# Kernel tuning notes

Measured on AMD Instinct MI355X. Metric: run time of the kernel, lower is better.

Reference implementation:

```python
import jax, jax.numpy as jnp
import numpy as np
import math

N_ENT = 200000
N_USERS = 100000
N_FACTORS = 4
N_REL = 26
CH = 64
N_EDGES = 1000000
NNZ = 1000000
KG_HEADS = 2


def scatter_softmax(scores, seg, num_segments):
    # numerically-stable softmax over groups defined by seg (per-head softmax)
    m = jax.ops.segment_max(scores, seg, num_segments=num_segments)
    m = jnp.where(jnp.isfinite(m), m, 0.0)
    e = jnp.exp(scores - m[seg])
    d = jax.ops.segment_sum(e, seg, num_segments=num_segments)
    return e / d[seg]


def setup_inputs() -> dict:
    key = jax.random.key(0)
    ks = jax.random.split(key, 11)
    return {
        "entity_emb": jax.random.normal(ks[0], (N_ENT, CH), dtype=jnp.float32) * 0.1,
        "user_emb": jax.random.normal(ks[1], (N_USERS, CH), dtype=jnp.float32) * 0.1,
        "latent_emb": jax.random.normal(ks[2], (N_FACTORS, CH), dtype=jnp.float32) * 0.1,
        "edge_index": jax.random.randint(ks[3], (2, N_EDGES), 0, N_ENT),
        "edge_type": jax.random.randint(ks[4], (N_EDGES,), 1, N_REL),  # in [1, N_REL-1]
        "ui_rows": jax.random.randint(ks[5], (NNZ,), 0, N_USERS),
        "ui_cols": jax.random.randint(ks[6], (NNZ,), 0, N_ENT),
        "ui_vals": jax.random.uniform(ks[7], (NNZ,), dtype=jnp.float32),
        "weight": jax.random.normal(ks[8], (N_REL - 1, CH), dtype=jnp.float32) * 0.1,
        "disen_weight_att": jax.random.normal(ks[9], (N_FACTORS, N_REL - 1), dtype=jnp.float32) * 0.1,
        "kg_W_r": jax.random.normal(ks[10], (CH, CH), dtype=jnp.float32) * (1.0 / math.sqrt(CH)),
    }


def reference(entity_emb, user_emb, latent_emb, edge_index, edge_type,
              ui_rows, ui_cols, ui_vals, weight, disen_weight_att, kg_W_r):
    head, tail = edge_index[0], edge_index[1]
    d_k = CH // KG_HEADS

    # --- Invariant_Capture.relation_aware_att ---
    rel_emb = weight[edge_type - 1]            # [E, C] gather
    h_emb = entity_emb[head]                   # [E, C] gather
    q = (h_emb @ kg_W_r).reshape(-1, KG_HEADS, d_k)
    k = (rel_emb @ kg_W_r).reshape(-1, KG_HEADS, d_k)
    score_r = ((q * k).sum(-1) / math.sqrt(d_k)).mean(-1)   # [E]
    rel_attn = scatter_softmax(score_r, head, N_ENT)

    # --- Invariant_Capture.kg_inv_capture ---
    t_emb = entity_emb[tail]                   # [E, C] gather
    r_emb = rel_emb * rel_attn[:, None]
    # bmm(cat(h,r), cat(t,r)^T) == h.t + r.r per edge
    score_trip = (h_emb * t_emb).sum(-1) + (r_emb * r_emb).sum(-1)
    kg_mask = scatter_softmax(score_trip, head, N_ENT)       # invariant_mask [E]

    # --- Aggregator: KG scatter-mean with invariant mask ---
    neigh = t_emb * rel_emb * kg_mask[:, None]               # [E, C]
    sums = jax.ops.segment_sum(neigh, head, num_segments=N_ENT)
    cnt = jax.ops.segment_sum(jnp.ones((neigh.shape[0],), dtype=neigh.dtype), head, num_segments=N_ENT)
    entity_agg = sums / jnp.maximum(cnt, 1.0)[:, None]       # scatter_mean

    # --- Aggregator: user side ---
    score = jax.nn.softmax(user_emb @ latent_emb.T, axis=1)  # [U, F]
    user_agg = jax.ops.segment_sum(entity_emb[ui_cols] * ui_vals[:, None], ui_rows, num_segments=N_USERS)
    disen_weight = jax.nn.softmax(disen_weight_att, axis=-1) @ weight  # [F, C]
    # (expand(U,F,C) * score[:,:,None]).sum(1) == score @ disen_weight
    user_agg = user_agg * (score @ disen_weight) + user_agg

    return jnp.concatenate([entity_agg, user_agg], axis=0)   # [N_ENT+N_USERS, C]
```

## Files before the change

kernel.cpp:

```cpp
#include <hip/hip_runtime.h>
#include <math.h>

#define N_ENT 200000
#define N_USERS 100000
#define NKEY 300000
#define N_FACTORS 4
#define NREL1 25
#define CH 64
#define N_EDGES 1000000
#define NNZ 1000000
#define NREC 2000000
#define BSHIFT 11
#define BKEYS 2048
#define NBUCKET 147
#define TILE 2048
#define CAP 24576
#define NCONVB ((N_ENT * 8 + 1023) / 1024)

#define SCORE_SCALE 0.08838834764831845f
#define INV_Q14 6.103888176768602e-05f

__device__ __forceinline__ float red8(float d) {
    d += __shfl_xor(d, 1);
    d += __shfl_xor(d, 2);
    d += __shfl_xor(d, 4);
    return d;
}
__device__ __forceinline__ float dot4(float4 a, float4 b) {
    return a.x * b.x + a.y * b.y + a.z * b.z + a.w * b.w;
}
__device__ __forceinline__ unsigned short f2bf(float f) {
    unsigned u = __float_as_uint(f);
    u += 0x7FFFu + ((u >> 16) & 1u);
    return (unsigned short)(u >> 16);
}
__device__ __forceinline__ float bf2f(unsigned short u) {
    return __uint_as_float(((unsigned)u) << 16);
}
__device__ __forceinline__ float4 bf4lo(uint4 t) {
    return make_float4(__uint_as_float(t.x << 16), __uint_as_float(t.x & 0xFFFF0000u),
                       __uint_as_float(t.y << 16), __uint_as_float(t.y & 0xFFFF0000u));
}
__device__ __forceinline__ float4 bf4hi(uint4 t) {
    return make_float4(__uint_as_float(t.z << 16), __uint_as_float(t.z & 0xFFFF0000u),
                       __uint_as_float(t.w << 16), __uint_as_float(t.w & 0xFFFF0000u));
}

__global__ void precompute_k(const float* __restrict__ W,
                             const float* __restrict__ weight,
                             const float* __restrict__ datt,
                             float* __restrict__ Mvec,
                             float* __restrict__ wnorm,
                             float* __restrict__ disen) {
    __shared__ float sW[64 * 64];
    __shared__ float sw[NREL1 * 64];
    __shared__ float sWWt[64 * 64];
    int tid = threadIdx.x;
    for (int i = tid; i < 64 * 64; i += 256) sW[i] = W[i];
    for (int i = tid; i < NREL1 * 64; i += 256) sw[i] = weight[i];
    __syncthreads();
    for (int e = tid; e < 64 * 64; e += 256) {
        int i = e >> 6, j = e & 63;
        float s = 0.f;
        for (int k = 0; k < 64; ++k) s += sW[i * 64 + k] * sW[j * 64 + k];
        sWWt[e] = s;
    }
    __syncthreads();
    for (int e = tid; e < NREL1 * 64; e += 256) {
        int r = e >> 6, i = e & 63;
        float s = 0.f;
        for (int j = 0; j < 64; ++j) s += sWWt[i * 64 + j] * sw[r * 64 + j];
        Mvec[e] = s;
    }
    for (int r = tid; r < NREL1; r += 256) {
        float s = 0.f;
        for (int j = 0; j < 64; ++j) { float v = sw[r * 64 + j]; s += v * v; }
        wnorm[r] = s;
    }
    for (int e = tid; e < N_FACTORS * 64; e += 256) {
        int f = e >> 6, c = e & 63;
        float m = -1e30f;
        for (int r = 0; r < NREL1; ++r) m = fmaxf(m, datt[f * NREL1 + r]);
        float ssum = 0.f, acc = 0.f;
        for (int r = 0; r < NREL1; ++r) {
            float p = expf(datt[f * NREL1 + r] - m);
            ssum += p;
            acc += p * sw[r * 64 + c];
        }
        disen[e] = acc / ssum;
    }
}

__global__ void binfill_k(const int* __restrict__ head, const int* __restrict__ tail,
                          const int* __restrict__ etype,
                          const int* __restrict__ rows, const int* __restrict__ cols,
                          const float* __restrict__ vals,
                          unsigned* __restrict__ gcur,
                          uint2* __restrict__ stg) {
    __shared__ unsigned hist[NBUCKET], base[NBUCKET], gbase[NBUCKET];
    __shared__ unsigned sh[256];
    __shared__ uint2 lrec[TILE];
    int tid = threadIdx.x;
    int tile0 = blockIdx.x * TILE;
    int tile_n = min(TILE, NREC - tile0);
    for (int b = tid; b < NBUCKET; b += 256) hist[b] = 0u;
    __syncthreads();
    unsigned key[8], pay[8], rank[8];
    for (int r = 0; r < 8; ++r) {
        int li = r * 256 + tid;
        key[r] = 0xFFFFFFFFu;
        if (li < tile_n) {
            int idx = tile0 + li;
            unsigned k, p;
            if (idx < N_EDGES) {
                k = (unsigned)head[idx];
                p = (unsigned)tail[idx] | ((unsigned)(etype[idx] - 1) << 18);
            } else {
                int j = idx - N_EDGES;
                k = (unsigned)(N_ENT + rows[j]);
                unsigned q = (unsigned)(vals[j] * 16383.f + 0.5f);
                p = (unsigned)cols[j] | (q << 18);
            }
            key[r] = k; pay[r] = p;
            rank[r] = atomicAdd(&hist[k >> BSHIFT], 1u);
        }
    }
    __syncthreads();
    unsigned v = (tid < NBUCKET) ? hist[tid] : 0u;
    sh[tid] = v; __syncthreads();
    for (int o = 1; o < 256; o <<= 1) {
        unsigned t = (tid >= o) ? sh[tid - o] : 0u;
        __syncthreads();
        sh[tid] += t;
        __syncthreads();
    }
    if (tid < NBUCKET) {
        base[tid] = sh[tid] - v;
        gbase[tid] = (unsigned)tid * CAP + (v ? atomicAdd(&gcur[tid], v) : 0u);
    }
    __syncthreads();
    for (int r = 0; r < 8; ++r) {
        if (key[r] != 0xFFFFFFFFu) {
            unsigned b = key[r] >> BSHIFT;
            unsigned pos = base[b] + rank[r];
            lrec[pos] = make_uint2(key[r], pay[r]);
        }
    }
    __syncthreads();
    for (int i = tid; i < tile_n; i += 256) {
        uint2 rec = lrec[i];
        unsigned b = rec.x >> BSHIFT;
        unsigned dst = gbase[b] + ((unsigned)i - base[b]);
        if (dst < (b + 1u) * CAP) stg[dst] = rec;
    }
}

__device__ __forceinline__
void place_bucket_dev(int b, int tid, const uint2* __restrict__ stg,
                      const unsigned* __restrict__ gcur,
                      unsigned* __restrict__ offs, unsigned* __restrict__ csr,
                      unsigned* shm) {
    unsigned c = (tid < NBUCKET) ? gcur[tid] : 0u;
    if (c > CAP) c = CAP;
    if (tid < 256) shm[tid] = c;
    __syncthreads();
    for (int o = 1; o < 256; o <<= 1) {
        unsigned t = (tid >= o && tid < 256) ? shm[tid - o] : 0u;
        __syncthreads();
        if (tid < 256) shm[tid] += t;
        __syncthreads();
    }
    if (tid == 0) {
        unsigned cb = gcur[b]; if (cb > CAP) cb = CAP;
        shm[3073] = cb;
        shm[3072] = shm[b] - cb;
        if (b == NBUCKET - 1) offs[NKEY] = shm[NBUCKET - 1];
    }
    __syncthreads();
    unsigned n = shm[3073], gb = shm[3072];
    const uint2* seg = stg + (size_t)b * CAP;
    unsigned* cnt = shm;
    unsigned* sc  = shm + 2048;
    cnt[tid * 2] = 0u; cnt[tid * 2 + 1] = 0u;
    __syncthreads();
    for (unsigned i = tid; i < n; i += 1024) {
        unsigned kk = seg[i].x - ((unsigned)b << BSHIFT);
        atomicAdd(&cnt[kk], 1u);
    }
    __syncthreads();
    unsigned c0 = cnt[tid * 2], c1 = cnt[tid * 2 + 1];
    unsigned tsum = c0 + c1;
    sc[tid] = tsum; __syncthreads();
    for (int o = 1; o < 1024; o <<= 1) {
        unsigned t = (tid >= o) ? sc[tid - o] : 0u;
        __syncthreads();
        sc[tid] += t;
        __syncthreads();
    }
    unsigned e0 = sc[tid] - tsum;
    unsigned e1 = e0 + c0;
    int k0 = (b << BSHIFT) + tid * 2;
    if (k0 < NKEY)     offs[k0]     = gb + e0;
    if (k0 + 1 < NKEY) offs[k0 + 1] = gb + e1;
    cnt[tid * 2] = e0; cnt[tid * 2 + 1] = e1;
    __syncthreads();
    for (unsigned i = tid; i < n; i += 1024) {
        uint2 rec = seg[i];
        unsigned kk = rec.x - ((unsigned)b << BSHIFT);
        unsigned pos = atomicAdd(&cnt[kk], 1u);
        csr[gb + pos] = rec.y;
    }
}

__device__ __forceinline__
void convE_dev(int cb, int tid, const float* __restrict__ ent,
               const float* __restrict__ Mvec,
               uint4* __restrict__ entb, unsigned short* __restrict__ E16,
               unsigned* shm) {
    float4* sM = (float4*)shm;
    for (int i = tid; i < NREL1 * 16; i += 1024) sM[i] = ((const float4*)Mvec)[i];
    __syncthreads();
    int idx = cb * 1024 + tid;
    int h = idx >> 3;
    int sub = tid & 7;
    if (h >= N_ENT) return;
    const float4* e4 = (const float4*)ent;
    float4 a = e4[h * 16 + sub * 2], b4 = e4[h * 16 + sub * 2 + 1];
    uint4 o;
    o.x = (unsigned)f2bf(a.x)  | ((unsigned)f2bf(a.y)  << 16);
    o.y = (unsigned)f2bf(a.z)  | ((unsigned)f2bf(a.w)  << 16);
    o.z = (unsigned)f2bf(b4.x) | ((unsigned)f2bf(b4.y) << 16);
    o.w = (unsigned)f2bf(b4.z) | ((unsigned)f2bf(b4.w) << 16);
    entb[h * 8 + sub] = o;
    for (int r = 0; r < NREL1; ++r) {
        float d = dot4(a, sM[r * 16 + sub * 2]) + dot4(b4, sM[r * 16 + sub * 2 + 1]);
        d = red8(d);
        if (sub == (r & 7)) E16[h * NREL1 + r] = f2bf(__expf(d * SCORE_SCALE));
    }
}

__global__ void binplace3_k(const uint2* __restrict__ stg,
                            const unsigned* __restrict__ gcur,
                            unsigned* __restrict__ offs,
                            unsigned* __restrict__ csr) {
    __shared__ __align__(16) unsigned shm[3074];
    place_bucket_dev(blockIdx.x, threadIdx.x, stg, gcur, offs, csr, shm);
}

__global__ void convE2_k(const float* __restrict__ ent,
                         const float* __restrict__ Mvec,
                         uint4* __restrict__ entb,
                         unsigned short* __restrict__ E16) {
    __shared__ __align__(16) unsigned shm[3074];
    convE_dev(blockIdx.x, threadIdx.x, ent, Mvec, entb, E16, shm);
}

__global__ void placeconv_k(const uint2* __restrict__ stg,
                            const unsigned* __restrict__ gcur,
                            unsigned* __restrict__ offs,
                            unsigned* __restrict__ csr,
                            const float* __restrict__ ent,
                            const float* __restrict__ Mvec,
                            uint4* __restrict__ entb,
                            unsigned short* __restrict__ E16) {
    __shared__ __align__(16) unsigned shm[3074];
    int b = blockIdx.x;
    if (b < NBUCKET)
        place_bucket_dev(b, threadIdx.x, stg, gcur, offs, csr, shm);
    else
        convE_dev(b - NBUCKET, threadIdx.x, ent, Mvec, entb, E16, shm);
}

template<bool FAST>
__global__ void gather8_k(const float* __restrict__ ent,
                          const uint4* __restrict__ entb,
                          const unsigned short* __restrict__ E16,
                          const float* __restrict__ weight,
                          const float* __restrict__ Mvec,
                          const float* __restrict__ wnorm,
                          const float* __restrict__ uemb,
                          const float* __restrict__ lat,
                          const float* __restrict__ disen,
                          const unsigned* __restrict__ offs,
                          const unsigned* __restrict__ csr,
                          float* __restrict__ out) {
    int gid = blockIdx.x * 256 + threadIdx.x;
    int key = gid >> 3;
    int sub = threadIdx.x & 7;
    if (key >= NKEY) return;
    unsigned beg = offs[key], end = offs[key + 1];
    const float4* e4 = (const float4*)ent;
    const float4* w4 = (const float4*)weight;
    float4* o4 = (float4*)out;
    const float4 z = make_float4(0.f, 0.f, 0.f, 0.f);

    if (key < N_ENT) {
        int h = key;
        if (beg == end) {
            o4[h * 16 + sub * 2] = z;
            o4[h * 16 + sub * 2 + 1] = z;
            return;
        }
        float4 hv0 = e4[h * 16 + sub * 2], hv1 = e4[h * 16 + sub * 2 + 1];
        float dr = 0.f;
        if (FAST) {
            for (unsigned i = beg + sub; i < end; i += 8)
                dr += bf2f(E16[h * NREL1 + (csr[i] >> 18)]);
            dr = red8(dr);
        } else {
            for (unsigned i = beg; i < end; ++i) {
                int r = csr[i] >> 18;
                float d = dot4(hv0, ((const float4*)Mvec)[r * 16 + sub * 2]) +
                          dot4(hv1, ((const float4*)Mvec)[r * 16 + sub * 2 + 1]);
                dr += __expf(red8(d) * SCORE_SCALE);
            }
        }
        float inv_dr = 1.0f / dr;
        float4 a0 = z, a1 = z;
        float dt = 0.f;
        unsigned i = beg;
        for (; i + 2 <= end; i += 2) {
            unsigned p0 = csr[i], p1 = csr[i + 1];
            int t0 = p0 & 0x3FFFF, r0 = p0 >> 18;
            int t1 = p1 & 0x3FFFF, r1 = p1 >> 18;
            float4 tv00, tv01, tv10, tv11;
            if (FAST) {
                uint4 tb0 = entb[t0 * 8 + sub];
                uint4 tb1 = entb[t1 * 8 + sub];
                tv00 = bf4lo(tb0); tv01 = bf4hi(tb0);
                tv10 = bf4lo(tb1); tv11 = bf4hi(tb1);
            } else {
                tv00 = e4[t0 * 16 + sub * 2]; tv01 = e4[t0 * 16 + sub * 2 + 1];
                tv10 = e4[t1 * 16 + sub * 2]; tv11 = e4[t1 * 16 + sub * 2 + 1];
            }
            float d0 = red8(dot4(hv0, tv00) + dot4(hv1, tv01));
            float d1 = red8(dot4(hv0, tv10) + dot4(hv1, tv11));
            float er0, er1;
            if (FAST) {
                er0 = bf2f(E16[h * NREL1 + r0]);
                er1 = bf2f(E16[h * NREL1 + r1]);
            } else {
                float q0 = dot4(hv0, ((const float4*)Mvec)[r0 * 16 + sub * 2]) +
                           dot4(hv1, ((const float4*)Mvec)[r0 * 16 + sub * 2 + 1]);
                float q1 = dot4(hv0, ((const float4*)Mvec)[r1 * 16 + sub * 2]) +
                           dot4(hv1, ((const float4*)Mvec)[r1 * 16 + sub * 2 + 1]);
                er0 = __expf(red8(q0) * SCORE_SCALE);
                er1 = __expf(red8(q1) * SCORE_SCALE);
            }
            float ra0 = er0 * inv_dr, ra1 = er1 * inv_dr;
            float et0 = __expf(d0 + ra0 * ra0 * wnorm[r0]);
            float et1 = __expf(d1 + ra1 * ra1 * wnorm[r1]);
            dt += et0 + et1;
            float4 wv;
            wv = w4[r0 * 16 + sub * 2];
            a0.x += et0 * tv00.x * wv.x; a0.y += et0 * tv00.y * wv.y;
            a0.z += et0 * tv00.z * wv.z; a0.w += et0 * tv00.w * wv.w;
            wv = w4[r0 * 16 + sub * 2 + 1];
            a1.x += et0 * tv01.x * wv.x; a1.y += et0 * tv01.y * wv.y;
            a1.z += et0 * tv01.z * wv.z; a1.w += et0 * tv01.w * wv.w;
            wv = w4[r1 * 16 + sub * 2];
            a0.x += et1 * tv10.x * wv.x; a0.y += et1 * tv10.y * wv.y;
            a0.z += et1 * tv10.z * wv.z; a0.w += et1 * tv10.w * wv.w;
            wv = w4[r1 * 16 + sub * 2 + 1];
            a1.x += et1 * tv11.x * wv.x; a1.y += et1 * tv11.y * wv.y;
            a1.z += et1 * tv11.z * wv.z; a1.w += et1 * tv11.w * wv.w;
        }
        if (i < end) {
            unsigned p = csr[i];
            int t = p & 0x3FFFF, r = p >> 18;
            float4 tv0, tv1;
            if (FAST) {
                uint4 tb = entb[t * 8 + sub];
                tv0 = bf4lo(tb); tv1 = bf4hi(tb);
            } else {
                tv0 = e4[t * 16 + sub * 2]; tv1 = e4[t * 16 + sub * 2 + 1];
            }
            float d = red8(dot4(hv0, tv0) + dot4(hv1, tv1));
            float er;
            if (FAST) {
                er = bf2f(E16[h * NREL1 + r]);
            } else {
                float q = dot4(hv0, ((const float4*)Mvec)[r * 16 + sub * 2]) +
                          dot4(hv1, ((const float4*)Mvec)[r * 16 + sub * 2 + 1]);
                er = __expf(red8(q) * SCORE_SCALE);
            }
            float ra = er * inv_dr;
            float et = __expf(d + ra * ra * wnorm[r]);
            dt += et;
            float4 wv;
            wv = w4[r * 16 + sub * 2];
            a0.x += et * tv0.x * wv.x; a0.y += et * tv0.y * wv.y;
            a0.z += et * tv0.z * wv.z; a0.w += et * tv0.w * wv.w;
            wv = w4[r * 16 + sub * 2 + 1];
            a1.x += et * tv1.x * wv.x; a1.y += et * tv1.y * wv.y;
            a1.z += et * tv1.z * wv.z; a1.w += et * tv1.w * wv.w;
        }
        float inv = 1.0f / (dt * (float)(end - beg));
        a0.x *= inv; a0.y *= inv; a0.z *= inv; a0.w *= inv;
        a1.x *= inv; a1.y *= inv; a1.z *= inv; a1.w *= inv;
        o4[h * 16 + sub * 2] = a0;
        o4[h * 16 + sub * 2 + 1] = a1;
    } else {
        int u = key - N_ENT;
        float4 a0 = z, a1 = z;
        unsigned i = beg;
        for (; i + 2 <= end; i += 2) {
            unsigned p0 = csr[i], p1 = csr[i + 1];
            int c0 = p0 & 0x3FFFF, c1 = p1 & 0x3FFFF;
            float v0 = (float)(p0 >> 18) * INV_Q14;
            float v1 = (float)(p1 >> 18) * INV_Q14;
            float4 tv00, tv01, tv10, tv11;
            if (FAST) {
                uint4 tb0 = entb[c0 * 8 + sub];
                uint4 tb1 = entb[c1 * 8 + sub];
                tv00 = bf4lo(tb0); tv01 = bf4hi(tb0);
                tv10 = bf4lo(tb1); tv11 = bf4hi(tb1);
            } else {
                tv00 = e4[c0 * 16 + sub * 2]; tv01 = e4[c0 * 16 + sub * 2 + 1];
                tv10 = e4[c1 * 16 + sub * 2]; tv11 = e4[c1 * 16 + sub * 2 + 1];
            }
            a0.x += v0 * tv00.x + v1 * tv10.x; a0.y += v0 * tv00.y + v1 * tv10.y;
            a0.z += v0 * tv00.z + v1 * tv10.z; a0.w += v0 * tv00.w + v1 * tv10.w;
            a1.x += v0 * tv01.x + v1 * tv11.x; a1.y += v0 * tv01.y + v1 * tv11.y;
            a1.z += v0 * tv01.z + v1 * tv11.z; a1.w += v0 * tv01.w + v1 * tv11.w;
        }
        if (i < end) {
            unsigned p = csr[i];
            int c = p & 0x3FFFF;
            float v = (float)(p >> 18) * INV_Q14;
            float4 tv0, tv1;
            if (FAST) {
                uint4 tb = entb[c * 8 + sub];
                tv0 = bf4lo(tb); tv1 = bf4hi(tb);
            } else {
                tv0 = e4[c * 16 + sub * 2]; tv1 = e4[c * 16 + sub * 2 + 1];
            }
            a0.x += v * tv0.x; a0.y += v * tv0.y; a0.z += v * tv0.z; a0.w += v * tv0.w;
            a1.x += v * tv1.x; a1.y += v * tv1.y; a1.z += v * tv1.z; a1.w += v * tv1.w;
        }
        float4 uv0 = ((const float4*)uemb)[u * 16 + sub * 2];
        float4 uv1 = ((const float4*)uemb)[u * 16 + sub * 2 + 1];
        float d[N_FACTORS];
        for (int f = 0; f < N_FACTORS; ++f) {
            float t = dot4(uv0, ((const float4*)lat)[f * 16 + sub * 2]) +
                      dot4(uv1, ((const float4*)lat)[f * 16 + sub * 2 + 1]);
            d[f] = red8(t);
        }
        float m = fmaxf(fmaxf(d[0], d[1]), fmaxf(d[2], d[3]));
        float s = 0.f, p_[N_FACTORS];
        for (int f = 0; f < N_FACTORS; ++f) { p_[f] = __expf(d[f] - m); s += p_[f]; }
        float invs = 1.0f / s;
        float4 g0 = z, g1 = z;
        for (int f = 0; f < N_FACTORS; ++f) {
            float w = p_[f] * invs;
            float4 dv = ((const float4*)disen)[f * 16 + sub * 2];
            g0.x += w * dv.x; g0.y += w * dv.y; g0.z += w * dv.z; g0.w += w * dv.w;
            dv = ((const float4*)disen)[f * 16 + sub * 2 + 1];
            g1.x += w * dv.x; g1.y += w * dv.y; g1.z += w * dv.z; g1.w += w * dv.w;
        }
        a0.x *= (1.0f + g0.x); a0.y *= (1.0f + g0.y);
        a0.z *= (1.0f + g0.z); a0.w *= (1.0f + g0.w);
        a1.x *= (1.0f + g1.x); a1.y *= (1.0f + g1.y);
        a1.z *= (1.0f + g1.z); a1.w *= (1.0f + g1.w);
        o4[key * 16 + sub * 2] = a0;
        o4[key * 16 + sub * 2 + 1] = a1;
    }
}

extern "C" void kernel_launch(void* const* d_in, const int* in_sizes, int n_in,
                              void* d_out, int out_size, void* d_ws, size_t ws_size,
                              hipStream_t stream) {
    (void)in_sizes; (void)n_in; (void)out_size;
    const float* ent    = (const float*)d_in[0];
    const float* uemb   = (const float*)d_in[1];
    const float* lat    = (const float*)d_in[2];
    const int*   eidx   = (const int*)d_in[3];
    const int*   etype  = (const int*)d_in[4];
    const int*   urows  = (const int*)d_in[5];
    const int*   ucols  = (const int*)d_in[6];
    const float* uvals  = (const float*)d_in[7];
    const float* weight = (const float*)d_in[8];
    const float* datt   = (const float*)d_in[9];
    const float* W      = (const float*)d_in[10];

    const int* head = eidx;
    const int* tail = eidx + N_EDGES;
    float* out = (float*)d_out;

    unsigned* gcur  = (unsigned*)d_ws;
    unsigned* offs  = gcur + 256;
    float*    Mvec  = (float*)(offs + NKEY + 2);
    float*    wnorm = Mvec + NREL1 * 64;
    float*    disen = wnorm + 32;
    unsigned* csr   = (unsigned*)(disen + N_FACTORS * 64);
    unsigned* big   = csr + NREC;

    size_t base_words = 256 + (NKEY + 2) + 1888 + (size_t)NREC;
    size_t stg_words  = (size_t)NBUCKET * CAP * 2;
    size_t tbl_words  = (size_t)N_ENT * 32 + ((size_t)N_ENT * NREL1 + 1) / 2;
    size_t big_alias  = stg_words > tbl_words ? stg_words : tbl_words;
    size_t need_fast     = (base_words + big_alias) * 4;
    size_t need_min      = (base_words + stg_words) * 4;
    size_t need_disjoint = (base_words + stg_words + tbl_words) * 4;
    bool fast     = ws_size >= need_fast;
    bool disjoint = ws_size >= need_disjoint;
    if (ws_size < need_min) return;

    uint2*    stg  = (uint2*)big;
    unsigned* entw = disjoint ? (big + stg_words) : big;
    uint4*    entb = (uint4*)entw;
    unsigned short* E16 = (unsigned short*)(entw + (size_t)N_ENT * 32);

    const int BLK = 256;

    hipMemsetAsync(gcur, 0, 256 * sizeof(unsigned), stream);
    precompute_k<<<1, 256, 0, stream>>>(W, weight, datt, Mvec, wnorm, disen);
    binfill_k<<<(NREC + TILE - 1) / TILE, BLK, 0, stream>>>(
        head, tail, etype, urows, ucols, uvals, gcur, stg);

    if (disjoint) {
        placeconv_k<<<NBUCKET + NCONVB, 1024, 0, stream>>>(
            stg, gcur, offs, csr, ent, Mvec, entb, E16);
    } else {
        binplace3_k<<<NBUCKET, 1024, 0, stream>>>(stg, gcur, offs, csr);
        if (fast)
            convE2_k<<<NCONVB, 1024, 0, stream>>>(ent, Mvec, entb, E16);
    }

    int gridG = (NKEY * 8 + BLK - 1) / BLK;
    if (fast) {
        gather8_k<true><<<gridG, BLK, 0, stream>>>(
            ent, entb, E16, weight, Mvec, wnorm,
            uemb, lat, disen, offs, csr, out);
    } else {
        gather8_k<false><<<gridG, BLK, 0, stream>>>(
            ent, entb, E16, weight, Mvec, wnorm,
            uemb, lat, disen, offs, csr, out);
    }
}
```

Baseline: 203.7 us.

## Scatter binfill records directly to global and load head rows as bf16

The binning kernel drops the shared-memory prefix scan and the local staging buffer. Each record is now written straight to its global bucket slot using the atomic rank from the histogram, which removes two barriers and the LDS round trip but makes the global stores less coalesced. In the FAST path, the aggregation kernel also reads the head entity vector from the packed bf16 copy instead of fp32. That halves the bytes loaded per head at some loss of precision.

```diff
diff --git a/kernel.cpp b/kernel.cpp
--- a/kernel.cpp
+++ b/kernel.cpp
@@ -97,9 +97,7 @@
                           const float* __restrict__ vals,
                           unsigned* __restrict__ gcur,
                           uint2* __restrict__ stg) {
-    __shared__ unsigned hist[NBUCKET], base[NBUCKET], gbase[NBUCKET];
-    __shared__ unsigned sh[256];
-    __shared__ uint2 lrec[TILE];
+    __shared__ unsigned hist[NBUCKET], gbase[NBUCKET];
     int tid = threadIdx.x;
     int tile0 = blockIdx.x * TILE;
     int tile_n = min(TILE, NREC - tile0);
@@ -126,32 +124,18 @@
         }
     }
     __syncthreads();
-    unsigned v = (tid < NBUCKET) ? hist[tid] : 0u;
-    sh[tid] = v; __syncthreads();
-    for (int o = 1; o < 256; o <<= 1) {
-        unsigned t = (tid >= o) ? sh[tid - o] : 0u;
-        __syncthreads();
-        sh[tid] += t;
-        __syncthreads();
-    }
     if (tid < NBUCKET) {
-        base[tid] = sh[tid] - v;
+        unsigned v = hist[tid];
         gbase[tid] = (unsigned)tid * CAP + (v ? atomicAdd(&gcur[tid], v) : 0u);
     }
     __syncthreads();
     for (int r = 0; r < 8; ++r) {
         if (key[r] != 0xFFFFFFFFu) {
             unsigned b = key[r] >> BSHIFT;
-            unsigned pos = base[b] + rank[r];
-            lrec[pos] = make_uint2(key[r], pay[r]);
-        }
-    }
-    __syncthreads();
-    for (int i = tid; i < tile_n; i += 256) {
-        uint2 rec = lrec[i];
-        unsigned b = rec.x >> BSHIFT;
-        unsigned dst = gbase[b] + ((unsigned)i - base[b]);
-        if (dst < (b + 1u) * CAP) stg[dst] = rec;
+            unsigned dst = gbase[b] + rank[r];
+            if (dst < (b + 1u) * CAP)
+                stg[dst] = make_uint2(key[r], pay[r]);
+        }
     }
 }
 
@@ -301,7 +285,13 @@
             o4[h * 16 + sub * 2 + 1] = z;
             return;
         }
-        float4 hv0 = e4[h * 16 + sub * 2], hv1 = e4[h * 16 + sub * 2 + 1];
+        float4 hv0, hv1;
+        if (FAST) {
+            uint4 hb = entb[h * 8 + sub];
+            hv0 = bf4lo(hb); hv1 = bf4hi(hb);
+        } else {
+            hv0 = e4[h * 16 + sub * 2]; hv1 = e4[h * 16 + sub * 2 + 1];
+        }
         float dr = 0.f;
         if (FAST) {
             for (unsigned i = beg + sub; i < end; i += 8)
```

New measurement: 202.0 us. No clear change (-0.8%).
